# Kernel tuning notes

Hardware: AMD Instinct MI355X
Metric: run time of the kernel (lower is better)

## Reference

```python
import jax, jax.numpy as jnp
import numpy as np

D = 1024          # n_embd
E = 8             # n_experts
FF = 4 * D        # ffn hidden
CAP = 2048        # expert_capacity
W_IMP = 0.01
W_LOAD = 0.01
LAMBDA_Z = 0.001
W_PEN = 0.01
B, S = 4, 2048
T = B * S


def setup_inputs() -> dict:
    key = jax.random.key(0)
    ks = jax.random.split(key, 8)
    x = jax.random.normal(ks[0], (B, S, D), dtype=jnp.float32)
    gate_w = jax.random.normal(ks[1], (E, D), dtype=jnp.float32) * 0.02   # Linear(D,E) weight
    w1 = jax.random.normal(ks[2], (E, D, FF), dtype=jnp.float32) * 0.02   # c_fc weight per expert
    b1 = jnp.zeros((E, FF), dtype=jnp.float32)
    w2 = jax.random.normal(ks[3], (E, FF, D), dtype=jnp.float32) * 0.02   # c_proj weight per expert
    b2 = jnp.zeros((E, D), dtype=jnp.float32)
    rnd = jax.random.uniform(ks[4], (T,), dtype=jnp.float32)              # torch.rand_like(g2)
    return {"x": x, "gate_w": gate_w, "w1": w1, "b1": b1, "w2": w2, "b2": b2, "rnd": rnd}


def _dispatch_ffn_combine(xf, e_ids, pos, wts, mask, w1, b1, w2, b2):
    """Capacity-buffered dispatch -> grouped FFN -> weighted combine for one routing slot.
    xf: [T,D]; e_ids: [T] int; pos: [T] position within expert; wts: [T] combine weight
    (already zeroed where masked); mask: [T] bool within-capacity (and stochastic) mask."""
    pc = jnp.clip(pos, 0, CAP - 1)
    buf = jnp.zeros((E, CAP, xf.shape[-1]), xf.dtype)
    # masked tokens contribute zeros; valid positions are unique per expert so add == set
    buf = buf.at[e_ids, pc].add(xf * mask[:, None].astype(xf.dtype))
    h = jax.nn.gelu(jnp.einsum('ecd,edf->ecf', buf, w1) + b1[:, None, :], approximate=True)
    out = jnp.einsum('ecf,efd->ecd', h, w2) + b2[:, None, :]          # [E,C,D]
    return out[e_ids, pc] * wts[:, None]                               # [T,D]


def _forward(x, gate_w, w1, b1, w2, b2, rnd):
    xf = x.reshape(-1, x.shape[-1])                                    # [T,D]
    logits = xf @ gate_w.T                                             # [T,E] (bias=False)

    # auxiliary losses
    p166 = jax.nn.softmax(logits / 1.66, axis=-1)
    penalty_a = jnp.mean(p166 * (1.0 - p166))
    pm = p166.mean(axis=0)
    penalty_b = 1.0 / E - jnp.mean(pm * (1.0 - pm))
    penalty = W_PEN * (penalty_a + penalty_b)
    z_loss = LAMBDA_Z * jnp.mean(jax.nn.logsumexp(logits, axis=-1) ** 2)

    probs = jax.nn.softmax(logits.astype(jnp.float32), axis=-1).astype(x.dtype)
    weights, sel = jax.lax.top_k(probs, 2)
    g1, g2 = weights[:, 0], weights[:, 1]
    e1, e2 = sel[:, 0], sel[:, 1]
    denom = g1 + g2
    g1n, g2n = g1 / denom, g2 / denom

    oh1 = jax.nn.one_hot(e1, E, dtype=jnp.int32)
    pos1 = jnp.take_along_axis(jnp.cumsum(oh1, axis=0), e1[:, None], axis=1)[:, 0] - 1
    mask1 = pos1 < CAP
    w_slot1 = g1n * mask1.astype(x.dtype)

    oh2 = jax.nn.one_hot(e2, E, dtype=jnp.int32)
    pos2 = jnp.take_along_axis(jnp.cumsum(oh2, axis=0), e2[:, None], axis=1)[:, 0] - 1
    mask2 = (pos2 < CAP) & (rnd < 2.0 * g2n)
    w_slot2 = g2n * mask2.astype(x.dtype)

    # load-balance loss: f_i from top-1 one-hot, P_i from softmax probs
    f_i = oh1.astype(jnp.float32).mean(axis=0)
    P_i = probs.mean(axis=0)
    load_loss = W_LOAD * E * jnp.sum(f_i * P_i)

    # importance loss over combine matrix G (column sums)
    imp = jnp.zeros((E,), x.dtype).at[e1].add(w_slot1).at[e2].add(w_slot2)
    mean = imp.mean()
    var = jnp.var(imp)
    imp_loss = W_IMP * var / (mean ** 2)

    aux = penalty + z_loss + load_loss + imp_loss

    y = _dispatch_ffn_combine(xf, e1, pos1, w_slot1, mask1, w1, b1, w2, b2)
    y = y + _dispatch_ffn_combine(xf, e2, pos2, w_slot2, mask2, w1, b1, w2, b2)
    return y.reshape(x.shape), aux


def reference(x, gate_w, w1, b1, w2, b2, rnd):
    return _forward(x, gate_w, w1, b1, w2, b2, rnd)
```

## Files before the change

kernel.cpp:

```cpp
#include <hip/hip_runtime.h>
#include <math.h>
#include <stdint.h>

#define DD 1024
#define EE 8
#define FF 4096
#define CAPV 2048
#define TT 8192
#define LIST_STRIDE 4096

typedef __bf16 bf16x8 __attribute__((ext_vector_type(8)));
typedef __bf16 bf16x4 __attribute__((ext_vector_type(4)));
typedef float floatx4 __attribute__((ext_vector_type(4)));

typedef __attribute__((address_space(3))) unsigned int as3_uint;
typedef __attribute__((address_space(1))) const unsigned int as1_uint;

__device__ __forceinline__ void gl_lds16(const void* g, void* l) {
    __builtin_amdgcn_global_load_lds((as1_uint*)g, (as3_uint*)l, 16, 0, 0);
}

__device__ __forceinline__ unsigned short f2bf(float f) {
    union { float f; unsigned int u; } v; v.f = f;
    const unsigned int r = v.u + 0x7FFFu + ((v.u >> 16) & 1u);
    return (unsigned short)(r >> 16);
}

__global__ __launch_bounds__(256) void moe_gate_kernel(
    const float* __restrict__ x, const float* __restrict__ gw,
    int* __restrict__ e1o, int* __restrict__ e2o,
    float* __restrict__ g1o, float* __restrict__ g2o,
    float* __restrict__ sums, __bf16* __restrict__ xb)
{
    __shared__ float sgw[EE][DD];
    __shared__ float wp[4][26];
    for (int i = threadIdx.x; i < EE * DD; i += 256) sgw[i >> 10][i & 1023] = gw[i];
    __syncthreads();

    const int wave = threadIdx.x >> 6, lane = threadIdx.x & 63;
    const int gwave = blockIdx.x * 4 + wave;
    const int nwaves = gridDim.x * 4;

    float pa_acc = 0.f, z_acc = 0.f;
    float P_acc[EE] = {0}, p6_acc[EE] = {0};
    int n1_acc[EE] = {0};

    for (int t = gwave; t < TT; t += nwaves) {
        float acc[EE] = {0};
        const float* xr = x + (size_t)t * DD;
        __bf16* xbr = xb + (size_t)t * DD;
        #pragma unroll
        for (int i = 0; i < DD / 64; ++i) {
            const float xv = xr[lane + 64 * i];
            xbr[lane + 64 * i] = (__bf16)xv;
            #pragma unroll
            for (int e = 0; e < EE; ++e) acc[e] += xv * sgw[e][lane + 64 * i];
        }
        #pragma unroll
        for (int e = 0; e < EE; ++e) {
            float v = acc[e];
            #pragma unroll
            for (int off = 32; off > 0; off >>= 1) v += __shfl_xor(v, off, 64);
            acc[e] = v;
        }
        if (lane == 0) {
            float mx = acc[0];
            #pragma unroll
            for (int e = 1; e < EE; ++e) mx = fmaxf(mx, acc[e]);
            float pr[EE], p6[EE], se = 0.f, s6 = 0.f;
            #pragma unroll
            for (int e = 0; e < EE; ++e) {
                pr[e] = __expf(acc[e] - mx); se += pr[e];
                p6[e] = __expf((acc[e] - mx) * (1.0f / 1.66f)); s6 += p6[e];
            }
            const float lse = mx + __logf(se);
            z_acc += lse * lse;
            const float ise = 1.f / se, is6 = 1.f / s6;
            #pragma unroll
            for (int e = 0; e < EE; ++e) {
                pr[e] *= ise; p6[e] *= is6;
                P_acc[e] += pr[e]; p6_acc[e] += p6[e];
                pa_acc += p6[e] * (1.f - p6[e]);
            }
            int a = 0;
            #pragma unroll
            for (int e = 1; e < EE; ++e) if (pr[e] > pr[a]) a = e;
            int b = (a == 0) ? 1 : 0;
            #pragma unroll
            for (int e = 0; e < EE; ++e) if (e != a && pr[e] > pr[b]) b = e;
            n1_acc[a]++;
            const float ga = pr[a], gb = pr[b], idn = 1.f / (ga + gb);
            e1o[t] = a; e2o[t] = b;
            g1o[t] = ga * idn; g2o[t] = gb * idn;
        }
    }
    if (lane == 0) {
        wp[wave][0] = pa_acc; wp[wave][1] = z_acc;
        #pragma unroll
        for (int e = 0; e < EE; ++e) {
            wp[wave][2 + e] = P_acc[e]; wp[wave][10 + e] = p6_acc[e];
            wp[wave][18 + e] = (float)n1_acc[e];
        }
    }
    __syncthreads();
    if (threadIdx.x < 26) {
        const float s = wp[0][threadIdx.x] + wp[1][threadIdx.x] + wp[2][threadIdx.x] + wp[3][threadIdx.x];
        atomicAdd(&sums[threadIdx.x], s);
    }
}

__global__ __launch_bounds__(256) void moe_scan_kernel(
    const int* __restrict__ e1i, const int* __restrict__ e2i,
    const float* __restrict__ g1i, const float* __restrict__ g2i,
    const float* __restrict__ rnd, const float* __restrict__ sums,
    int* __restrict__ etok, int* __restrict__ p1o, int* __restrict__ p2o,
    int* __restrict__ cnt1, int* __restrict__ cnt2,
    float* __restrict__ imp1, float* __restrict__ imp2)
{
    const int bid = blockIdx.x, slot = bid >> 3, e = bid & 7;
    const int tid = threadIdx.x, wave = tid >> 6, lane = tid & 63;
    __shared__ int wtA[4], wtB[4];
    __shared__ float red[256];
    const int* ev = slot ? e2i : e1i;
    const float* gv = slot ? g2i : g1i;
    int* po = slot ? p2o : p1o;
    const int base = slot ? min((int)sums[18 + e], CAPV) : 0;

    int runTot = 0, runM = 0;
    float limp = 0.f;
    for (int c = 0; c < TT / 256; ++c) {
        const int t = c * 256 + tid;
        const int sel = (ev[t] == e) ? 1 : 0;
        const float w = gv[t];
        int ps = sel;
        #pragma unroll
        for (int off = 1; off < 64; off <<= 1) { int v = __shfl_up(ps, off, 64); if (lane >= off) ps += v; }
        if (lane == 63) wtA[wave] = ps;
        __syncthreads();
        int wpre = 0, ctot = 0;
        #pragma unroll
        for (int ww = 0; ww < 4; ++ww) { if (ww < wave) wpre += wtA[ww]; ctot += wtA[ww]; }
        const int pos = runTot + wpre + ps - 1;
        int m, idx;
        if (slot == 0) {
            m = sel && (pos < CAPV);
            idx = pos;
        } else {
            m = (sel && (pos < CAPV) && (rnd[t] < 2.f * w)) ? 1 : 0;
            int pm = m;
            #pragma unroll
            for (int off = 1; off < 64; off <<= 1) { int v = __shfl_up(pm, off, 64); if (lane >= off) pm += v; }
            if (lane == 63) wtB[wave] = pm;
            __syncthreads();
            int wpm = 0, mtot = 0;
            #pragma unroll
            for (int ww = 0; ww < 4; ++ww) { if (ww < wave) wpm += wtB[ww]; mtot += wtB[ww]; }
            idx = runM + wpm + pm - 1;
            runM += mtot;
        }
        if (sel) po[t] = m ? (e * LIST_STRIDE + base + idx) : -1;
        if (m) {
            etok[e * LIST_STRIDE + base + idx] = t;
            limp += w;
        }
        runTot += ctot;
        __syncthreads();
    }
    red[tid] = limp; __syncthreads();
    for (int s = 128; s > 0; s >>= 1) { if (tid < s) red[tid] += red[tid + s]; __syncthreads(); }
    if (tid == 0) {
        if (slot == 0) { cnt1[e] = min(runTot, CAPV); imp1[e] = red[0]; }
        else           { cnt2[e] = runM;              imp2[e] = red[0]; }
    }
}

__global__ void moe_aux_kernel(const float* __restrict__ sums,
                               const float* __restrict__ imp1, const float* __restrict__ imp2,
                               float* __restrict__ out_aux)
{
    if (threadIdx.x != 0 || blockIdx.x != 0) return;
    const float invT = 1.f / (float)TT;
    const float pa = sums[0] / ((float)TT * (float)EE);
    float pb = 0.f, load = 0.f, msum = 0.f;
    float im[EE];
    for (int e = 0; e < EE; ++e) {
        const float pm = sums[10 + e] * invT;
        pb += pm * (1.f - pm);
        load += (sums[18 + e] * invT) * (sums[2 + e] * invT);
        im[e] = imp1[e] + imp2[e];
        msum += im[e];
    }
    pb = 1.f / (float)EE - pb / (float)EE;
    const float penalty = 0.01f * (pa + pb);
    const float z_loss = 0.001f * sums[1] * invT;
    const float load_loss = 0.01f * (float)EE * load;
    const float mean = msum / (float)EE;
    float var = 0.f;
    for (int e = 0; e < EE; ++e) { const float d = im[e] - mean; var += d * d; }
    var /= (float)EE;
    const float imp_loss = 0.01f * var / (mean * mean);
    *out_aux = penalty + z_loss + load_loss + imp_loss;
}

__global__ __launch_bounds__(256) void transpose_bf16_kernel(
    const float* __restrict__ in, __bf16* __restrict__ out, int K, int N)
{
    __shared__ float tile[32][65];
    const int e = blockIdx.z;
    const float* ine = in + (size_t)e * K * N;
    __bf16* oute = out + (size_t)e * K * N;
    const int bk = blockIdx.x * 64, bn = blockIdx.y * 32;
    const int tid = threadIdx.x;
    #pragma unroll
    for (int p = 0; p < 8; ++p) {
        const int idx = p * 256 + tid;
        const int kl = idx >> 5, nl = idx & 31;
        tile[nl][kl] = ine[(size_t)(bk + kl) * N + bn + nl];
    }
    __syncthreads();
    #pragma unroll
    for (int p = 0; p < 4; ++p) {
        const int wdx = p * 256 + tid;
        const int nl = wdx >> 5, c = wdx & 31;
        const unsigned int pk = (unsigned int)f2bf(tile[nl][c * 2])
                              | ((unsigned int)f2bf(tile[nl][c * 2 + 1]) << 16);
        *(unsigned int*)&oute[(size_t)(bn + nl) * K + bk + c * 2] = pk;
    }
}

__global__ __launch_bounds__(512, 2) void moe_ffn1_mfma(
    const __bf16* __restrict__ xb, const __bf16* __restrict__ w1T,
    const float* __restrict__ b1, const int* __restrict__ etok,
    const int* __restrict__ cnt1, const int* __restrict__ cnt2,
    __bf16* __restrict__ H)
{
    const int f = blockIdx.x;
    const int xcd = f & 7, s = f >> 3;
    const int g = xcd * 16 + (s >> 4);
    const int e = g >> 4, n0 = (g & 15) * 256;
    const int m0 = (s & 15) * 256;
    const int ce = cnt1[e] + cnt2[e];
    if (m0 >= ce) return;
    const int tid = threadIdx.x, lane = tid & 63, w = tid >> 6;
    const int wm = w >> 2, wn = w & 3;
    const int quad = lane >> 4, l16 = lane & 15;

    __shared__ __bf16 As[2][16384];
    __shared__ __bf16 Bs[2][16384];

    const int srow = tid >> 3;
    const int srcoff = ((tid & 7) ^ (srow & 7)) * 8;
    const __bf16* ap[4];
    const __bf16* bp[4];
    const __bf16* bbase = w1T + (size_t)e * FF * DD;
    #pragma unroll
    for (int r = 0; r < 4; ++r) {
        const int gr = m0 + r * 64 + srow;
        const int tok = (gr < ce) ? etok[e * LIST_STRIDE + gr] : 0;
        ap[r] = xb + (size_t)tok * DD + srcoff;
        bp[r] = bbase + (size_t)(n0 + r * 64 + srow) * DD + srcoff;
    }
    const int ldst = w * 512;

    floatx4 acc[8][4];
    #pragma unroll
    for (int i = 0; i < 8; ++i)
        #pragma unroll
        for (int j = 0; j < 4; ++j) acc[i][j] = floatx4{0.f, 0.f, 0.f, 0.f};

    const int abase  = (wm * 128 + l16) * 64;
    const int bbase2 = (wn * 64 + l16) * 64;
    const int sw0 = (quad ^ (l16 & 7)) * 8;
    const int sw1 = ((4 + quad) ^ (l16 & 7)) * 8;

    auto stage = [&](int bufi, int koff) {
        #pragma unroll
        for (int r = 0; r < 4; ++r)
            gl_lds16(ap[r] + koff, &As[bufi][r * 4096 + ldst]);
        #pragma unroll
        for (int r = 0; r < 4; ++r)
            gl_lds16(bp[r] + koff, &Bs[bufi][r * 4096 + ldst]);
    };
    auto compute = [&](int bufi) {
        bf16x8 bfr[4][2];
        #pragma unroll
        for (int j = 0; j < 4; ++j) {
            bfr[j][0] = *(const bf16x8*)&Bs[bufi][bbase2 + j * 1024 + sw0];
            bfr[j][1] = *(const bf16x8*)&Bs[bufi][bbase2 + j * 1024 + sw1];
        }
        #pragma unroll
        for (int mh = 0; mh < 2; ++mh) {
            bf16x8 av[4][2];
            #pragma unroll
            for (int i2 = 0; i2 < 4; ++i2) {
                av[i2][0] = *(const bf16x8*)&As[bufi][abase + (mh * 4 + i2) * 1024 + sw0];
                av[i2][1] = *(const bf16x8*)&As[bufi][abase + (mh * 4 + i2) * 1024 + sw1];
            }
            #pragma unroll
            for (int i2 = 0; i2 < 4; ++i2)
                #pragma unroll
                for (int j = 0; j < 4; ++j) {
                    floatx4 c = acc[mh * 4 + i2][j];
                    c = __builtin_amdgcn_mfma_f32_16x16x32_bf16(bfr[j][0], av[i2][0], c, 0, 0, 0);
                    c = __builtin_amdgcn_mfma_f32_16x16x32_bf16(bfr[j][1], av[i2][1], c, 0, 0, 0);
                    acc[mh * 4 + i2][j] = c;
                }
        }
    };

    stage(0, 0);
    stage(1, 64);
    asm volatile("s_waitcnt vmcnt(8)" ::: "memory");
    __builtin_amdgcn_s_barrier();

    #pragma unroll 2
    for (int t = 0; t < 16; ++t) {
        const int cur = t & 1;
        compute(cur);
        asm volatile("s_waitcnt lgkmcnt(0)" ::: "memory");
        __builtin_amdgcn_s_barrier();
        if (t < 14) {
            stage(cur, (t + 2) * 64);
            asm volatile("s_waitcnt vmcnt(8)" ::: "memory");
        } else {
            asm volatile("s_waitcnt vmcnt(0)" ::: "memory");
        }
        __builtin_amdgcn_s_barrier();
    }

    const float* b1e = b1 + (size_t)e * FF;
    #pragma unroll
    for (int i = 0; i < 8; ++i) {
        const int mrow = m0 + wm * 128 + i * 16 + l16;
        __bf16* hrow = H + ((size_t)e * LIST_STRIDE + mrow) * FF;
        #pragma unroll
        for (int j = 0; j < 4; ++j) {
            const int col0 = n0 + wn * 64 + j * 16 + quad * 4;
            const float4 bb = *(const float4*)&b1e[col0];
            float vv[4] = {acc[i][j][0] + bb.x, acc[i][j][1] + bb.y,
                           acc[i][j][2] + bb.z, acc[i][j][3] + bb.w};
            bf16x4 pk;
            #pragma unroll
            for (int r = 0; r < 4; ++r) {
                const float v = vv[r];
                const float u = 0.7978845608028654f * (v + 0.044715f * v * v * v);
                const float th = 1.f - 2.f / (__expf(2.f * u) + 1.f);
                pk[r] = (__bf16)(0.5f * v * (1.f + th));
            }
            *(bf16x4*)&hrow[col0] = pk;
        }
    }
}

__global__ __launch_bounds__(512, 2) void moe_ffn2_mfma(
    const __bf16* __restrict__ H, const __bf16* __restrict__ w2T,
    const float* __restrict__ b2, const int* __restrict__ cnt1,
    const int* __restrict__ cnt2, __bf16* __restrict__ O)
{
    const int f = blockIdx.x;
    const int xcd = f & 7, s = f >> 3;
    const int g = xcd * 4 + (s >> 4);
    const int e = g >> 2, n0 = (g & 3) * 256;
    const int m0 = (s & 15) * 256;
    const int ce = cnt1[e] + cnt2[e];
    if (m0 >= ce) return;
    const int tid = threadIdx.x, lane = tid & 63, w = tid >> 6;
    const int wm = w >> 2, wn = w & 3;
    const int quad = lane >> 4, l16 = lane & 15;

    __shared__ __bf16 As[2][16384];
    __shared__ __bf16 Bs[2][16384];

    const int srow = tid >> 3;
    const int srcoff = ((tid & 7) ^ (srow & 7)) * 8;
    const __bf16* ap[4];
    const __bf16* bp[4];
    const __bf16* bbase = w2T + (size_t)e * DD * FF;
    #pragma unroll
    for (int r = 0; r < 4; ++r) {
        ap[r] = H + ((size_t)e * LIST_STRIDE + m0 + r * 64 + srow) * FF + srcoff;
        bp[r] = bbase + (size_t)(n0 + r * 64 + srow) * FF + srcoff;
    }
    const int ldst = w * 512;

    floatx4 acc[8][4];
    #pragma unroll
    for (int i = 0; i < 8; ++i)
        #pragma unroll
        for (int j = 0; j < 4; ++j) acc[i][j] = floatx4{0.f, 0.f, 0.f, 0.f};

    const int abase  = (wm * 128 + l16) * 64;
    const int bbase2 = (wn * 64 + l16) * 64;
    const int sw0 = (quad ^ (l16 & 7)) * 8;
    const int sw1 = ((4 + quad) ^ (l16 & 7)) * 8;

    auto stage = [&](int bufi, int koff) {
        #pragma unroll
        for (int r = 0; r < 4; ++r)
            gl_lds16(ap[r] + koff, &As[bufi][r * 4096 + ldst]);
        #pragma unroll
        for (int r = 0; r < 4; ++r)
            gl_lds16(bp[r] + koff, &Bs[bufi][r * 4096 + ldst]);
    };
    auto compute = [&](int bufi) {
        bf16x8 bfr[4][2];
        #pragma unroll
        for (int j = 0; j < 4; ++j) {
            bfr[j][0] = *(const bf16x8*)&Bs[bufi][bbase2 + j * 1024 + sw0];
            bfr[j][1] = *(const bf16x8*)&Bs[bufi][bbase2 + j * 1024 + sw1];
        }
        #pragma unroll
        for (int mh = 0; mh < 2; ++mh) {
            bf16x8 av[4][2];
            #pragma unroll
            for (int i2 = 0; i2 < 4; ++i2) {
                av[i2][0] = *(const bf16x8*)&As[bufi][abase + (mh * 4 + i2) * 1024 + sw0];
                av[i2][1] = *(const bf16x8*)&As[bufi][abase + (mh * 4 + i2) * 1024 + sw1];
            }
            #pragma unroll
            for (int i2 = 0; i2 < 4; ++i2)
                #pragma unroll
                for (int j = 0; j < 4; ++j) {
                    floatx4 c = acc[mh * 4 + i2][j];
                    c = __builtin_amdgcn_mfma_f32_16x16x32_bf16(bfr[j][0], av[i2][0], c, 0, 0, 0);
                    c = __builtin_amdgcn_mfma_f32_16x16x32_bf16(bfr[j][1], av[i2][1], c, 0, 0, 0);
                    acc[mh * 4 + i2][j] = c;
                }
        }
    };

    stage(0, 0);
    stage(1, 64);
    asm volatile("s_waitcnt vmcnt(8)" ::: "memory");
    __builtin_amdgcn_s_barrier();

    #pragma unroll 2
    for (int t = 0; t < 64; ++t) {
        const int cur = t & 1;
        compute(cur);
        asm volatile("s_waitcnt lgkmcnt(0)" ::: "memory");
        __builtin_amdgcn_s_barrier();
        if (t < 62) {
            stage(cur, (t + 2) * 64);
            asm volatile("s_waitcnt vmcnt(8)" ::: "memory");
        } else {
            asm volatile("s_waitcnt vmcnt(0)" ::: "memory");
        }
        __builtin_amdgcn_s_barrier();
    }

    const float* b2e = b2 + (size_t)e * DD;
    #pragma unroll
    for (int i = 0; i < 8; ++i) {
        const int grow = m0 + wm * 128 + i * 16 + l16;
        if (grow < ce) {
            __bf16* orow = O + ((size_t)e * LIST_STRIDE + grow) * DD;
            #pragma unroll
            for (int j = 0; j < 4; ++j) {
                const int col0 = n0 + wn * 64 + j * 16 + quad * 4;
                const float4 bb = *(const float4*)&b2e[col0];
                bf16x4 pk;
                pk[0] = (__bf16)(acc[i][j][0] + bb.x);
                pk[1] = (__bf16)(acc[i][j][1] + bb.y);
                pk[2] = (__bf16)(acc[i][j][2] + bb.z);
                pk[3] = (__bf16)(acc[i][j][3] + bb.w);
                *(bf16x4*)&orow[col0] = pk;
            }
        }
    }
}

__global__ __launch_bounds__(256) void moe_combine_kernel(
    const __bf16* __restrict__ O, const float* __restrict__ g1v,
    const float* __restrict__ g2v, const int* __restrict__ p1v,
    const int* __restrict__ p2v, float* __restrict__ y)
{
    const int t = blockIdx.x;
    const int col = threadIdx.x * 4;
    const int p1 = p1v[t], p2 = p2v[t];
    float4 r = make_float4(0.f, 0.f, 0.f, 0.f);
    if (p1 >= 0) {
        const float g = g1v[t];
        const bf16x4 v = *(const bf16x4*)&O[(size_t)p1 * DD + col];
        r.x += g * (float)v[0]; r.y += g * (float)v[1];
        r.z += g * (float)v[2]; r.w += g * (float)v[3];
    }
    if (p2 >= 0) {
        const float g = g2v[t];
        const bf16x4 v = *(const bf16x4*)&O[(size_t)p2 * DD + col];
        r.x += g * (float)v[0]; r.y += g * (float)v[1];
        r.z += g * (float)v[2]; r.w += g * (float)v[3];
    }
    *(float4*)&y[(size_t)t * DD + col] = r;
}

extern "C" void kernel_launch(void* const* d_in, const int* in_sizes, int n_in,
                              void* d_out, int out_size, void* d_ws, size_t ws_size,
                              hipStream_t stream) {
    const float* x   = (const float*)d_in[0];
    const float* gw  = (const float*)d_in[1];
    const float* w1  = (const float*)d_in[2];
    const float* b1  = (const float*)d_in[3];
    const float* w2  = (const float*)d_in[4];
    const float* b2  = (const float*)d_in[5];
    const float* rnd = (const float*)d_in[6];
    float* out = (float*)d_out;

    char* p = (char*)d_ws;
    float* sums = (float*)p;
    float* imp1 = (float*)(p + 128);
    float* imp2 = (float*)(p + 160);
    int*   cnt1 = (int*)(p + 192);
    int*   cnt2 = (int*)(p + 224);
    p += 512;
    int*   e1v = (int*)p;   p += TT * 4;
    int*   e2v = (int*)p;   p += TT * 4;
    float* g1v = (float*)p; p += TT * 4;
    float* g2v = (float*)p; p += TT * 4;
    int*   p1v = (int*)p;   p += TT * 4;
    int*   p2v = (int*)p;   p += TT * 4;
    int*   etok = (int*)p;  p += EE * LIST_STRIDE * 4;
    uintptr_t q = (((uintptr_t)p) + 255) & ~(uintptr_t)255;
    __bf16* xb  = (__bf16*)q;  q += (size_t)TT * DD * 2;
    __bf16* w1T = (__bf16*)q;  q += (size_t)EE * FF * DD * 2;
    __bf16* w2T = (__bf16*)q;  q += (size_t)EE * DD * FF * 2;
    __bf16* H   = (__bf16*)q;  q += (size_t)EE * LIST_STRIDE * FF * 2;
    __bf16* O   = (__bf16*)q;

    hipMemsetAsync(sums, 0, 128, stream);

    moe_gate_kernel<<<256, 256, 0, stream>>>(x, gw, e1v, e2v, g1v, g2v, sums, xb);
    moe_scan_kernel<<<16, 256, 0, stream>>>(e1v, e2v, g1v, g2v, rnd, sums,
                                            etok, p1v, p2v, cnt1, cnt2, imp1, imp2);
    moe_aux_kernel<<<1, 64, 0, stream>>>(sums, imp1, imp2, out + (size_t)TT * DD);

    transpose_bf16_kernel<<<dim3(DD / 64, FF / 32, EE), 256, 0, stream>>>(w1, w1T, DD, FF);
    transpose_bf16_kernel<<<dim3(FF / 64, DD / 32, EE), 256, 0, stream>>>(w2, w2T, FF, DD);

    moe_ffn1_mfma<<<2048, 512, 0, stream>>>(xb, w1T, b1, etok, cnt1, cnt2, H);
    moe_ffn2_mfma<<<512, 512, 0, stream>>>(H, w2T, b2, cnt1, cnt2, O);
    moe_combine_kernel<<<TT, 256, 0, stream>>>(O, g1v, g2v, p1v, p2v, out);
}
```

Baseline: 711.6 us.

## Interleave fine-grained global-to-LDS staging with MFMA sub-phases in FFN K-loops

Replaces the coarse stage-then-compute double-buffered K loop in both expert FFN GEMM kernels with a four-phase schedule. Each phase issues a couple of global_load_lds transfers for the next tiles, loads one K-half of the A/B fragments, and runs 16 MFMAs at raised wave priority (s_setprio). The goal is to spread memory traffic across the compute, keep fewer LDS fragments live, and hide load latency better. It adds many more barriers per iteration and relies on the vmcnt accounting being correct; the clamped tail prefetches issue redundant loads.

```diff
diff --git a/kernel.cpp b/kernel.cpp
--- a/kernel.cpp
+++ b/kernel.cpp
@@ -228,6 +228,91 @@
     }
 }
 
+#define FFN_KLOOP(NT)                                                          \
+                \
+    stA(0,0,0); stA(0,2,0); stB(0,0,0); stB(0,1,0);                            \
+    stA(0,1,0); stA(0,3,0); stB(0,2,0); stB(0,3,0);                            \
+    stA(1,0,1); stA(1,2,1); stB(1,0,1); stB(1,1,1);                            \
+    _Pragma("unroll 2")                                                        \
+    for (int t = 0; t < (NT); ++t) {                                           \
+        const int c = t & 1, o = c ^ 1;                                        \
+        const int u1 = (t + 1 < (NT)) ? t + 1 : (NT) - 1;                      \
+        const int u2 = (t + 2 < (NT)) ? t + 2 : (NT) - 1;                      \
+        bf16x8 bfr[4][2], av[4];                                               \
+                                            \
+        stA(o, 1, u1); stA(o, 3, u1);                                          \
+        asm volatile("s_waitcnt vmcnt(4)" ::: "memory");                       \
+        __builtin_amdgcn_s_barrier();                                          \
+        _Pragma("unroll")                                                      \
+        for (int j = 0; j < 4; ++j)                                            \
+            bfr[j][0] = *(const bf16x8*)&Bs[c][bbase2 + j * 1024 + sw0];       \
+        _Pragma("unroll")                                                      \
+        for (int i = 0; i < 4; ++i)                                            \
+            av[i] = *(const bf16x8*)&As[c][abase + i * 1024 + sw0];            \
+        __builtin_amdgcn_s_setprio(1);                                         \
+        _Pragma("unroll")                                                      \
+        for (int i = 0; i < 4; ++i)                                            \
+            _Pragma("unroll")                                                  \
+            for (int j = 0; j < 4; ++j)                                        \
+                acc[i][j] = __builtin_amdgcn_mfma_f32_16x16x32_bf16(           \
+                    bfr[j][0], av[i], acc[i][j], 0, 0, 0);                     \
+        __builtin_amdgcn_s_setprio(0);                                         \
+        asm volatile("s_waitcnt lgkmcnt(0)" ::: "memory");                     \
+        __builtin_amdgcn_s_barrier();                                          \
+                                            \
+        stB(o, 2, u1); stB(o, 3, u1);                                          \
+        _Pragma("unroll")                                                      \
+        for (int j = 0; j < 4; ++j)                                            \
+            bfr[j][1] = *(const bf16x8*)&Bs[c][bbase2 + j * 1024 + sw1];       \
+        _Pragma("unroll")                                                      \
+        for (int i = 0; i < 4; ++i)                                            \
+            av[i] = *(const bf16x8*)&As[c][abase + i * 1024 + sw1];            \
+        __builtin_amdgcn_s_barrier();                                          \
+        __builtin_amdgcn_s_setprio(1);                                         \
+        _Pragma("unroll")                                                      \
+        for (int i = 0; i < 4; ++i)                                            \
+            _Pragma("unroll")                                                  \
+            for (int j = 0; j < 4; ++j)                                        \
+                acc[i][j] = __builtin_amdgcn_mfma_f32_16x16x32_bf16(           \
+                    bfr[j][1], av[i], acc[i][j], 0, 0, 0);                     \
+        __builtin_amdgcn_s_setprio(0);                                         \
+        asm volatile("s_waitcnt lgkmcnt(0)" ::: "memory");                     \
+        __builtin_amdgcn_s_barrier();        \
+                                            \
+        stA(c, 0, u2); stA(c, 2, u2);                                          \
+        _Pragma("unroll")                                                      \
+        for (int i = 0; i < 4; ++i)                                            \
+            av[i] = *(const bf16x8*)&As[c][abase + (4 + i) * 1024 + sw0];      \
+        __builtin_amdgcn_s_barrier();                                          \
+        __builtin_amdgcn_s_setprio(1);                                         \
+        _Pragma("unroll")                                                      \
+        for (int i = 0; i < 4; ++i)                                            \
+            _Pragma("unroll")                                                  \
+            for (int j = 0; j < 4; ++j)                                        \
+                acc[4 + i][j] = __builtin_amdgcn_mfma_f32_16x16x32_bf16(       \
+                    bfr[j][0], av[i], acc[4 + i][j], 0, 0, 0);                 \
+        __builtin_amdgcn_s_setprio(0);                                         \
+        asm volatile("s_waitcnt lgkmcnt(0)" ::: "memory");                     \
+        __builtin_amdgcn_s_barrier();                                          \
+                                            \
+        stB(c, 0, u2); stB(c, 1, u2);                                          \
+        _Pragma("unroll")                                                      \
+        for (int i = 0; i < 4; ++i)                                            \
+            av[i] = *(const bf16x8*)&As[c][abase + (4 + i) * 1024 + sw1];      \
+        __builtin_amdgcn_s_barrier();                                          \
+        __builtin_amdgcn_s_setprio(1);                                         \
+        _Pragma("unroll")                                                      \
+        for (int i = 0; i < 4; ++i)                                            \
+            _Pragma("unroll")                                                  \
+            for (int j = 0; j < 4; ++j)                                        \
+                acc[4 + i][j] = __builtin_amdgcn_mfma_f32_16x16x32_bf16(       \
+                    bfr[j][1], av[i], acc[4 + i][j], 0, 0, 0);                 \
+        __builtin_amdgcn_s_setprio(0);                                         \
+        asm volatile("s_waitcnt lgkmcnt(0)" ::: "memory");                     \
+        __builtin_amdgcn_s_barrier();                                          \
+    }                                                                          \
+    asm volatile("s_waitcnt vmcnt(0)" ::: "memory");
+
 __global__ __launch_bounds__(512, 2) void moe_ffn1_mfma(
     const __bf16* __restrict__ xb, const __bf16* __restrict__ w1T,
     const float* __restrict__ b1, const int* __restrict__ etok,
@@ -273,60 +358,10 @@
     const int sw0 = (quad ^ (l16 & 7)) * 8;
     const int sw1 = ((4 + quad) ^ (l16 & 7)) * 8;
 
-    auto stage = [&](int bufi, int koff) {
-        #pragma unroll
-        for (int r = 0; r < 4; ++r)
-            gl_lds16(ap[r] + koff, &As[bufi][r * 4096 + ldst]);
-        #pragma unroll
-        for (int r = 0; r < 4; ++r)
-            gl_lds16(bp[r] + koff, &Bs[bufi][r * 4096 + ldst]);
-    };
-    auto compute = [&](int bufi) {
-        bf16x8 bfr[4][2];
-        #pragma unroll
-        for (int j = 0; j < 4; ++j) {
-            bfr[j][0] = *(const bf16x8*)&Bs[bufi][bbase2 + j * 1024 + sw0];
-            bfr[j][1] = *(const bf16x8*)&Bs[bufi][bbase2 + j * 1024 + sw1];
-        }
-        #pragma unroll
-        for (int mh = 0; mh < 2; ++mh) {
-            bf16x8 av[4][2];
-            #pragma unroll
-            for (int i2 = 0; i2 < 4; ++i2) {
-                av[i2][0] = *(const bf16x8*)&As[bufi][abase + (mh * 4 + i2) * 1024 + sw0];
-                av[i2][1] = *(const bf16x8*)&As[bufi][abase + (mh * 4 + i2) * 1024 + sw1];
-            }
-            #pragma unroll
-            for (int i2 = 0; i2 < 4; ++i2)
-                #pragma unroll
-                for (int j = 0; j < 4; ++j) {
-                    floatx4 c = acc[mh * 4 + i2][j];
-                    c = __builtin_amdgcn_mfma_f32_16x16x32_bf16(bfr[j][0], av[i2][0], c, 0, 0, 0);
-                    c = __builtin_amdgcn_mfma_f32_16x16x32_bf16(bfr[j][1], av[i2][1], c, 0, 0, 0);
-                    acc[mh * 4 + i2][j] = c;
-                }
-        }
-    };
-
-    stage(0, 0);
-    stage(1, 64);
-    asm volatile("s_waitcnt vmcnt(8)" ::: "memory");
-    __builtin_amdgcn_s_barrier();
-
-    #pragma unroll 2
-    for (int t = 0; t < 16; ++t) {
-        const int cur = t & 1;
-        compute(cur);
-        asm volatile("s_waitcnt lgkmcnt(0)" ::: "memory");
-        __builtin_amdgcn_s_barrier();
-        if (t < 14) {
-            stage(cur, (t + 2) * 64);
-            asm volatile("s_waitcnt vmcnt(8)" ::: "memory");
-        } else {
-            asm volatile("s_waitcnt vmcnt(0)" ::: "memory");
-        }
-        __builtin_amdgcn_s_barrier();
-    }
+    auto stA = [&](int buf, int r, int u) { gl_lds16(ap[r] + u * 64, &As[buf][r * 4096 + ldst]); };
+    auto stB = [&](int buf, int r, int u) { gl_lds16(bp[r] + u * 64, &Bs[buf][r * 4096 + ldst]); };
+
+    FFN_KLOOP(16)
 
     const float* b1e = b1 + (size_t)e * FF;
     #pragma unroll
@@ -394,60 +429,10 @@
     const int sw0 = (quad ^ (l16 & 7)) * 8;
     const int sw1 = ((4 + quad) ^ (l16 & 7)) * 8;
 
-    auto stage = [&](int bufi, int koff) {
-        #pragma unroll
-        for (int r = 0; r < 4; ++r)
-            gl_lds16(ap[r] + koff, &As[bufi][r * 4096 + ldst]);
-        #pragma unroll
-        for (int r = 0; r < 4; ++r)
-            gl_lds16(bp[r] + koff, &Bs[bufi][r * 4096 + ldst]);
-    };
-    auto compute = [&](int bufi) {
-        bf16x8 bfr[4][2];
-        #pragma unroll
-        for (int j = 0; j < 4; ++j) {
-            bfr[j][0] = *(const bf16x8*)&Bs[bufi][bbase2 + j * 1024 + sw0];
-            bfr[j][1] = *(const bf16x8*)&Bs[bufi][bbase2 + j * 1024 + sw1];
-        }
-        #pragma unroll
-        for (int mh = 0; mh < 2; ++mh) {
-            bf16x8 av[4][2];
-            #pragma unroll
-            for (int i2 = 0; i2 < 4; ++i2) {
-                av[i2][0] = *(const bf16x8*)&As[bufi][abase + (mh * 4 + i2) * 1024 + sw0];
-                av[i2][1] = *(const bf16x8*)&As[bufi][abase + (mh * 4 + i2) * 1024 + sw1];
-            }
-            #pragma unroll
-            for (int i2 = 0; i2 < 4; ++i2)
-                #pragma unroll
-                for (int j = 0; j < 4; ++j) {
-                    floatx4 c = acc[mh * 4 + i2][j];
-                    c = __builtin_amdgcn_mfma_f32_16x16x32_bf16(bfr[j][0], av[i2][0], c, 0, 0, 0);
-                    c = __builtin_amdgcn_mfma_f32_16x16x32_bf16(bfr[j][1], av[i2][1], c, 0, 0, 0);
-                    acc[mh * 4 + i2][j] = c;
-                }
-        }
-    };
-
-    stage(0, 0);
-    stage(1, 64);
-    asm volatile("s_waitcnt vmcnt(8)" ::: "memory");
-    __builtin_amdgcn_s_barrier();
-
-    #pragma unroll 2
-    for (int t = 0; t < 64; ++t) {
-        const int cur = t & 1;
-        compute(cur);
-        asm volatile("s_waitcnt lgkmcnt(0)" ::: "memory");
-        __builtin_amdgcn_s_barrier();
-        if (t < 62) {
-            stage(cur, (t + 2) * 64);
-            asm volatile("s_waitcnt vmcnt(8)" ::: "memory");
-        } else {
-            asm volatile("s_waitcnt vmcnt(0)" ::: "memory");
-        }
-        __builtin_amdgcn_s_barrier();
-    }
+    auto stA = [&](int buf, int r, int u) { gl_lds16(ap[r] + u * 64, &As[buf][r * 4096 + ldst]); };
+    auto stB = [&](int buf, int r, int u) { gl_lds16(bp[r] + u * 64, &Bs[buf][r * 4096 + ldst]); };
+
+    FFN_KLOOP(64)
 
     const float* b2e = b2 + (size_t)e * DD;
     #pragma unroll
```

Result: slower. 746.1 us (+4.8%).

## Switch FFN GEMMs to 32x32x16 MFMA and fuse weight transposes into gate kernel

Applied to the files above, without the earlier changes.

The two expert FFN GEMM kernels now use 32x32x16 bf16 MFMA instructions with floatx16 accumulators instead of pairs of 16x16x32 ops. This roughly halves the LDS fragment loads per FLOP and raises s_setprio around the MFMA bursts. Separately, the gate kernel and both weight transpose kernels are merged into one launch by dispatching on block index, so the transposes can overlap the gating work and two launches go away. The epilogue index mapping is rewritten for the 32x32 output layout, which risks layout bugs, and the larger LDS allocation in the merged kernel may reduce occupancy for the transpose blocks.

```diff
diff --git a/kernel.cpp b/kernel.cpp
--- a/kernel.cpp
+++ b/kernel.cpp
@@ -12,6 +12,7 @@
 typedef __bf16 bf16x8 __attribute__((ext_vector_type(8)));
 typedef __bf16 bf16x4 __attribute__((ext_vector_type(4)));
 typedef float floatx4 __attribute__((ext_vector_type(4)));
+typedef float floatx16 __attribute__((ext_vector_type(16)));
 
 typedef __attribute__((address_space(3))) unsigned int as3_uint;
 typedef __attribute__((address_space(1))) const unsigned int as1_uint;
@@ -26,20 +27,67 @@
     return (unsigned short)(r >> 16);
 }
 
-__global__ __launch_bounds__(256) void moe_gate_kernel(
+#define GATE_BLOCKS 256
+#define T1_BLOCKS 16384
+#define T2_BLOCKS 16384
+
+__device__ __forceinline__ void transpose_body(
+    const float* __restrict__ in, __bf16* __restrict__ out,
+    int K, int N, int bk, int bn, int e, float (*tile)[65], int tid)
+{
+    const float* ine = in + (size_t)e * K * N;
+    __bf16* oute = out + (size_t)e * K * N;
+    #pragma unroll
+    for (int p = 0; p < 8; ++p) {
+        const int idx = p * 256 + tid;
+        const int kl = idx >> 5, nl = idx & 31;
+        tile[nl][kl] = ine[(size_t)(bk + kl) * N + bn + nl];
+    }
+    __syncthreads();
+    #pragma unroll
+    for (int p = 0; p < 4; ++p) {
+        const int wdx = p * 256 + tid;
+        const int nl = wdx >> 5, c = wdx & 31;
+        const unsigned int pk = (unsigned int)f2bf(tile[nl][c * 2])
+                              | ((unsigned int)f2bf(tile[nl][c * 2 + 1]) << 16);
+        *(unsigned int*)&oute[(size_t)(bn + nl) * K + bk + c * 2] = pk;
+    }
+}
+
+__global__ __launch_bounds__(256) void moe_prep_kernel(
     const float* __restrict__ x, const float* __restrict__ gw,
     int* __restrict__ e1o, int* __restrict__ e2o,
     float* __restrict__ g1o, float* __restrict__ g2o,
-    float* __restrict__ sums, __bf16* __restrict__ xb)
-{
-    __shared__ float sgw[EE][DD];
+    float* __restrict__ sums, __bf16* __restrict__ xb,
+    const float* __restrict__ w1, __bf16* __restrict__ w1T,
+    const float* __restrict__ w2, __bf16* __restrict__ w2T)
+{
+    __shared__ float smem[EE * DD];
     __shared__ float wp[4][26];
-    for (int i = threadIdx.x; i < EE * DD; i += 256) sgw[i >> 10][i & 1023] = gw[i];
+    const int bid = blockIdx.x;
+    const int tid = threadIdx.x;
+
+    if (bid >= GATE_BLOCKS) {
+        float (*tile)[65] = (float (*)[65])smem;
+        if (bid < GATE_BLOCKS + T1_BLOCKS) {
+            const int f = bid - GATE_BLOCKS;
+            transpose_body(w1, w1T, DD, FF, (f & 15) * 64, ((f >> 4) & 127) * 32,
+                           f >> 11, tile, tid);
+        } else {
+            const int f = bid - GATE_BLOCKS - T1_BLOCKS;
+            transpose_body(w2, w2T, FF, DD, (f & 63) * 64, ((f >> 6) & 31) * 32,
+                           f >> 11, tile, tid);
+        }
+        return;
+    }
+
+    float (*sgw)[DD] = (float (*)[DD])smem;
+    for (int i = tid; i < EE * DD; i += 256) sgw[i >> 10][i & 1023] = gw[i];
     __syncthreads();
 
-    const int wave = threadIdx.x >> 6, lane = threadIdx.x & 63;
-    const int gwave = blockIdx.x * 4 + wave;
-    const int nwaves = gridDim.x * 4;
+    const int wave = tid >> 6, lane = tid & 63;
+    const int gwave = bid * 4 + wave;
+    const int nwaves = GATE_BLOCKS * 4;
 
     float pa_acc = 0.f, z_acc = 0.f;
     float P_acc[EE] = {0}, p6_acc[EE] = {0};
@@ -103,9 +151,9 @@
         }
     }
     __syncthreads();
-    if (threadIdx.x < 26) {
-        const float s = wp[0][threadIdx.x] + wp[1][threadIdx.x] + wp[2][threadIdx.x] + wp[3][threadIdx.x];
-        atomicAdd(&sums[threadIdx.x], s);
+    if (tid < 26) {
+        const float s = wp[0][tid] + wp[1][tid] + wp[2][tid] + wp[3][tid];
+        atomicAdd(&sums[tid], s);
     }
 }
 
@@ -202,31 +250,42 @@
     *out_aux = penalty + z_loss + load_loss + imp_loss;
 }
 
-__global__ __launch_bounds__(256) void transpose_bf16_kernel(
-    const float* __restrict__ in, __bf16* __restrict__ out, int K, int N)
-{
-    __shared__ float tile[32][65];
-    const int e = blockIdx.z;
-    const float* ine = in + (size_t)e * K * N;
-    __bf16* oute = out + (size_t)e * K * N;
-    const int bk = blockIdx.x * 64, bn = blockIdx.y * 32;
-    const int tid = threadIdx.x;
-    #pragma unroll
-    for (int p = 0; p < 8; ++p) {
-        const int idx = p * 256 + tid;
-        const int kl = idx >> 5, nl = idx & 31;
-        tile[nl][kl] = ine[(size_t)(bk + kl) * N + bn + nl];
-    }
-    __syncthreads();
-    #pragma unroll
-    for (int p = 0; p < 4; ++p) {
-        const int wdx = p * 256 + tid;
-        const int nl = wdx >> 5, c = wdx & 31;
-        const unsigned int pk = (unsigned int)f2bf(tile[nl][c * 2])
-                              | ((unsigned int)f2bf(tile[nl][c * 2 + 1]) << 16);
-        *(unsigned int*)&oute[(size_t)(bn + nl) * K + bk + c * 2] = pk;
-    }
-}
+#define FFN_CORE32(NT)                                                         \
+    stage(0, 0);                                                               \
+    stage(1, 64);                                                              \
+    asm volatile("s_waitcnt vmcnt(8)" ::: "memory");                           \
+    __builtin_amdgcn_s_barrier();                                              \
+    for (int t = 0; t < (NT); ++t) {                                           \
+        const int cur = t & 1;                                                 \
+        _Pragma("unroll")                                                      \
+        for (int ks = 0; ks < 4; ++ks) {                                       \
+            bf16x8 av[4], bv[2];                                               \
+            const int ch = ((ks * 2 + hi) ^ kx) * 8;                           \
+            _Pragma("unroll")                                                  \
+            for (int mi = 0; mi < 4; ++mi)                                     \
+                av[mi] = *(const bf16x8*)&As[cur][ar[mi] + ch];                 \
+            _Pragma("unroll")                                                  \
+            for (int nj = 0; nj < 2; ++nj)                                     \
+                bv[nj] = *(const bf16x8*)&Bs[cur][br[nj] + ch];                 \
+            __builtin_amdgcn_s_setprio(1);                                     \
+            _Pragma("unroll")                                                  \
+            for (int mi = 0; mi < 4; ++mi)                                     \
+                _Pragma("unroll")                                              \
+                for (int nj = 0; nj < 2; ++nj)                                 \
+                    acc[mi][nj] = __builtin_amdgcn_mfma_f32_32x32x16_bf16(     \
+                        bv[nj], av[mi], acc[mi][nj], 0, 0, 0);                 \
+            __builtin_amdgcn_s_setprio(0);                                     \
+        }                                                                      \
+        asm volatile("s_waitcnt lgkmcnt(0)" ::: "memory");                     \
+        __builtin_amdgcn_s_barrier();                                          \
+        if (t < (NT) - 2) {                                                    \
+            stage(cur, (t + 2) * 64);                                          \
+            asm volatile("s_waitcnt vmcnt(8)" ::: "memory");                   \
+        } else {                                                               \
+            asm volatile("s_waitcnt vmcnt(0)" ::: "memory");                   \
+        }                                                                      \
+        __builtin_amdgcn_s_barrier();                                          \
+    }
 
 __global__ __launch_bounds__(512, 2) void moe_ffn1_mfma(
     const __bf16* __restrict__ xb, const __bf16* __restrict__ w1T,
@@ -243,7 +302,8 @@
     if (m0 >= ce) return;
     const int tid = threadIdx.x, lane = tid & 63, w = tid >> 6;
     const int wm = w >> 2, wn = w & 3;
-    const int quad = lane >> 4, l16 = lane & 15;
+    const int l32 = lane & 31, hi = lane >> 5;
+    const int kx = l32 & 7;
 
     __shared__ __bf16 As[2][16384];
     __shared__ __bf16 Bs[2][16384];
@@ -262,16 +322,19 @@
     }
     const int ldst = w * 512;
 
-    floatx4 acc[8][4];
-    #pragma unroll
-    for (int i = 0; i < 8; ++i)
-        #pragma unroll
-        for (int j = 0; j < 4; ++j) acc[i][j] = floatx4{0.f, 0.f, 0.f, 0.f};
-
-    const int abase  = (wm * 128 + l16) * 64;
-    const int bbase2 = (wn * 64 + l16) * 64;
-    const int sw0 = (quad ^ (l16 & 7)) * 8;
-    const int sw1 = ((4 + quad) ^ (l16 & 7)) * 8;
+    floatx16 acc[4][2];
+    #pragma unroll
+    for (int i = 0; i < 4; ++i)
+        #pragma unroll
+        for (int j = 0; j < 2; ++j)
+            #pragma unroll
+            for (int q = 0; q < 16; ++q) acc[i][j][q] = 0.f;
+
+    int ar[4], br[2];
+    #pragma unroll
+    for (int mi = 0; mi < 4; ++mi) ar[mi] = (wm * 128 + mi * 32 + l32) * 64;
+    #pragma unroll
+    for (int nj = 0; nj < 2; ++nj) br[nj] = (wn * 64 + nj * 32 + l32) * 64;
 
     auto stage = [&](int bufi, int koff) {
         #pragma unroll
@@ -281,74 +344,34 @@
         for (int r = 0; r < 4; ++r)
             gl_lds16(bp[r] + koff, &Bs[bufi][r * 4096 + ldst]);
     };
-    auto compute = [&](int bufi) {
-        bf16x8 bfr[4][2];
-        #pragma unroll
-        for (int j = 0; j < 4; ++j) {
-            bfr[j][0] = *(const bf16x8*)&Bs[bufi][bbase2 + j * 1024 + sw0];
-            bfr[j][1] = *(const bf16x8*)&Bs[bufi][bbase2 + j * 1024 + sw1];
-        }
-        #pragma unroll
-        for (int mh = 0; mh < 2; ++mh) {
-            bf16x8 av[4][2];
-            #pragma unroll
-            for (int i2 = 0; i2 < 4; ++i2) {
-                av[i2][0] = *(const bf16x8*)&As[bufi][abase + (mh * 4 + i2) * 1024 + sw0];
-                av[i2][1] = *(const bf16x8*)&As[bufi][abase + (mh * 4 + i2) * 1024 + sw1];
+
+    FFN_CORE32(16)
+
+    const float* b1e = b1 + (size_t)e * FF;
+    #pragma unroll
+    for (int mi = 0; mi < 4; ++mi) {
+        const int mrow = m0 + wm * 128 + mi * 32 + l32;
+        __bf16* hrow = H + ((size_t)e * LIST_STRIDE + mrow) * FF;
+        #pragma unroll
+        for (int nj = 0; nj < 2; ++nj)
+            #pragma unroll
+            for (int rg = 0; rg < 4; ++rg) {
+                const int col0 = n0 + wn * 64 + nj * 32 + rg * 8 + hi * 4;
+                const float4 bb = *(const float4*)&b1e[col0];
+                float vv[4] = {acc[mi][nj][rg * 4 + 0] + bb.x,
+                               acc[mi][nj][rg * 4 + 1] + bb.y,
+                               acc[mi][nj][rg * 4 + 2] + bb.z,
+                               acc[mi][nj][rg * 4 + 3] + bb.w};
+                bf16x4 pk;
+                #pragma unroll
+                for (int r = 0; r < 4; ++r) {
+                    const float v = vv[r];
+                    const float u = 0.7978845608028654f * (v + 0.044715f * v * v * v);
+                    const float th = 1.f - 2.f / (__expf(2.f * u) + 1.f);
+                    pk[r] = (__bf16)(0.5f * v * (1.f + th));
+                }
+                *(bf16x4*)&hrow[col0] = pk;
             }
-            #pragma unroll
-            for (int i2 = 0; i2 < 4; ++i2)
-                #pragma unroll
-                for (int j = 0; j < 4; ++j) {
-                    floatx4 c = acc[mh * 4 + i2][j];
-                    c = __builtin_amdgcn_mfma_f32_16x16x32_bf16(bfr[j][0], av[i2][0], c, 0, 0, 0);
-                    c = __builtin_amdgcn_mfma_f32_16x16x32_bf16(bfr[j][1], av[i2][1], c, 0, 0, 0);
-                    acc[mh * 4 + i2][j] = c;
-                }
-        }
-    };
-
-    stage(0, 0);
-    stage(1, 64);
-    asm volatile("s_waitcnt vmcnt(8)" ::: "memory");
-    __builtin_amdgcn_s_barrier();
-
-    #pragma unroll 2
-    for (int t = 0; t < 16; ++t) {
-        const int cur = t & 1;
-        compute(cur);
-        asm volatile("s_waitcnt lgkmcnt(0)" ::: "memory");
-        __builtin_amdgcn_s_barrier();
-        if (t < 14) {
-            stage(cur, (t + 2) * 64);
-            asm volatile("s_waitcnt vmcnt(8)" ::: "memory");
-        } else {
-            asm volatile("s_waitcnt vmcnt(0)" ::: "memory");
-        }
-        __builtin_amdgcn_s_barrier();
-    }
-
-    const float* b1e = b1 + (size_t)e * FF;
-    #pragma unroll
-    for (int i = 0; i < 8; ++i) {
-        const int mrow = m0 + wm * 128 + i * 16 + l16;
-        __bf16* hrow = H + ((size_t)e * LIST_STRIDE + mrow) * FF;
-        #pragma unroll
-        for (int j = 0; j < 4; ++j) {
-            const int col0 = n0 + wn * 64 + j * 16 + quad * 4;
-            const float4 bb = *(const float4*)&b1e[col0];
-            float vv[4] = {acc[i][j][0] + bb.x, acc[i][j][1] + bb.y,
-                           acc[i][j][2] + bb.z, acc[i][j][3] + bb.w};
-            bf16x4 pk;
-            #pragma unroll
-            for (int r = 0; r < 4; ++r) {
-                const float v = vv[r];
-                const float u = 0.7978845608028654f * (v + 0.044715f * v * v * v);
-                const float th = 1.f - 2.f / (__expf(2.f * u) + 1.f);
-                pk[r] = (__bf16)(0.5f * v * (1.f + th));
-            }
-            *(bf16x4*)&hrow[col0] = pk;
-        }
     }
 }
 
@@ -366,7 +389,8 @@
     if (m0 >= ce) return;
     const int tid = threadIdx.x, lane = tid & 63, w = tid >> 6;
     const int wm = w >> 2, wn = w & 3;
-    const int quad = lane >> 4, l16 = lane & 15;
+    const int l32 = lane & 31, hi = lane >> 5;
+    const int kx = l32 & 7;
 
     __shared__ __bf16 As[2][16384];
     __shared__ __bf16 Bs[2][16384];
@@ -383,16 +407,19 @@
     }
     const int ldst = w * 512;
 
-    floatx4 acc[8][4];
-    #pragma unroll
-    for (int i = 0; i < 8; ++i)
-        #pragma unroll
-        for (int j = 0; j < 4; ++j) acc[i][j] = floatx4{0.f, 0.f, 0.f, 0.f};
-
-    const int abase  = (wm * 128 + l16) * 64;
-    const int bbase2 = (wn * 64 + l16) * 64;
-    const int sw0 = (quad ^ (l16 & 7)) * 8;
-    const int sw1 = ((4 + quad) ^ (l16 & 7)) * 8;
+    floatx16 acc[4][2];
+    #pragma unroll
+    for (int i = 0; i < 4; ++i)
+        #pragma unroll
+        for (int j = 0; j < 2; ++j)
+            #pragma unroll
+            for (int q = 0; q < 16; ++q) acc[i][j][q] = 0.f;
+
+    int ar[4], br[2];
+    #pragma unroll
+    for (int mi = 0; mi < 4; ++mi) ar[mi] = (wm * 128 + mi * 32 + l32) * 64;
+    #pragma unroll
+    for (int nj = 0; nj < 2; ++nj) br[nj] = (wn * 64 + nj * 32 + l32) * 64;
 
     auto stage = [&](int bufi, int koff) {
         #pragma unroll
@@ -402,70 +429,28 @@
         for (int r = 0; r < 4; ++r)
             gl_lds16(bp[r] + koff, &Bs[bufi][r * 4096 + ldst]);
     };
-    auto compute = [&](int bufi) {
-        bf16x8 bfr[4][2];
-        #pragma unroll
-        for (int j = 0; j < 4; ++j) {
-            bfr[j][0] = *(const bf16x8*)&Bs[bufi][bbase2 + j * 1024 + sw0];
-            bfr[j][1] = *(const bf16x8*)&Bs[bufi][bbase2 + j * 1024 + sw1];
-        }
-        #pragma unroll
-        for (int mh = 0; mh < 2; ++mh) {
-            bf16x8 av[4][2];
-            #pragma unroll
-            for (int i2 = 0; i2 < 4; ++i2) {
-                av[i2][0] = *(const bf16x8*)&As[bufi][abase + (mh * 4 + i2) * 1024 + sw0];
-                av[i2][1] = *(const bf16x8*)&As[bufi][abase + (mh * 4 + i2) * 1024 + sw1];
-            }
-            #pragma unroll
-            for (int i2 = 0; i2 < 4; ++i2)
-                #pragma unroll
-                for (int j = 0; j < 4; ++j) {
-                    floatx4 c = acc[mh * 4 + i2][j];
-                    c = __builtin_amdgcn_mfma_f32_16x16x32_bf16(bfr[j][0], av[i2][0], c, 0, 0, 0);
-                    c = __builtin_amdgcn_mfma_f32_16x16x32_bf16(bfr[j][1], av[i2][1], c, 0, 0, 0);
-                    acc[mh * 4 + i2][j] = c;
-                }
-        }
-    };
-
-    stage(0, 0);
-    stage(1, 64);
-    asm volatile("s_waitcnt vmcnt(8)" ::: "memory");
-    __builtin_amdgcn_s_barrier();
-
-    #pragma unroll 2
-    for (int t = 0; t < 64; ++t) {
-        const int cur = t & 1;
-        compute(cur);
-        asm volatile("s_waitcnt lgkmcnt(0)" ::: "memory");
-        __builtin_amdgcn_s_barrier();
-        if (t < 62) {
-            stage(cur, (t + 2) * 64);
-            asm volatile("s_waitcnt vmcnt(8)" ::: "memory");
-        } else {
-            asm volatile("s_waitcnt vmcnt(0)" ::: "memory");
-        }
-        __builtin_amdgcn_s_barrier();
-    }
+
+    FFN_CORE32(64)
 
     const float* b2e = b2 + (size_t)e * DD;
     #pragma unroll
-    for (int i = 0; i < 8; ++i) {
-        const int grow = m0 + wm * 128 + i * 16 + l16;
+    for (int mi = 0; mi < 4; ++mi) {
+        const int grow = m0 + wm * 128 + mi * 32 + l32;
         if (grow < ce) {
             __bf16* orow = O + ((size_t)e * LIST_STRIDE + grow) * DD;
             #pragma unroll
-            for (int j = 0; j < 4; ++j) {
-                const int col0 = n0 + wn * 64 + j * 16 + quad * 4;
-                const float4 bb = *(const float4*)&b2e[col0];
-                bf16x4 pk;
-                pk[0] = (__bf16)(acc[i][j][0] + bb.x);
-                pk[1] = (__bf16)(acc[i][j][1] + bb.y);
-                pk[2] = (__bf16)(acc[i][j][2] + bb.z);
-                pk[3] = (__bf16)(acc[i][j][3] + bb.w);
-                *(bf16x4*)&orow[col0] = pk;
-            }
+            for (int nj = 0; nj < 2; ++nj)
+                #pragma unroll
+                for (int rg = 0; rg < 4; ++rg) {
+                    const int col0 = n0 + wn * 64 + nj * 32 + rg * 8 + hi * 4;
+                    const float4 bb = *(const float4*)&b2e[col0];
+                    bf16x4 pk;
+                    pk[0] = (__bf16)(acc[mi][nj][rg * 4 + 0] + bb.x);
+                    pk[1] = (__bf16)(acc[mi][nj][rg * 4 + 1] + bb.y);
+                    pk[2] = (__bf16)(acc[mi][nj][rg * 4 + 2] + bb.z);
+                    pk[3] = (__bf16)(acc[mi][nj][rg * 4 + 3] + bb.w);
+                    *(bf16x4*)&orow[col0] = pk;
+                }
         }
     }
 }
@@ -529,14 +514,12 @@
 
     hipMemsetAsync(sums, 0, 128, stream);
 
-    moe_gate_kernel<<<256, 256, 0, stream>>>(x, gw, e1v, e2v, g1v, g2v, sums, xb);
+    moe_prep_kernel<<<GATE_BLOCKS + T1_BLOCKS + T2_BLOCKS, 256, 0, stream>>>(
+        x, gw, e1v, e2v, g1v, g2v, sums, xb, w1, w1T, w2, w2T);
     moe_scan_kernel<<<16, 256, 0, stream>>>(e1v, e2v, g1v, g2v, rnd, sums,
                                             etok, p1v, p2v, cnt1, cnt2, imp1, imp2);
     moe_aux_kernel<<<1, 64, 0, stream>>>(sums, imp1, imp2, out + (size_t)TT * DD);
 
-    transpose_bf16_kernel<<<dim3(DD / 64, FF / 32, EE), 256, 0, stream>>>(w1, w1T, DD, FF);
-    transpose_bf16_kernel<<<dim3(FF / 64, DD / 32, EE), 256, 0, stream>>>(w2, w2T, FF, DD);
-
     moe_ffn1_mfma<<<2048, 512, 0, stream>>>(xb, w1T, b1, etok, cnt1, cnt2, H);
     moe_ffn2_mfma<<<512, 512, 0, stream>>>(H, w2T, b2, cnt1, cnt2, O);
     moe_combine_kernel<<<TT, 256, 0, stream>>>(O, g1v, g2v, p1v, p2v, out);
```

Measured after the change: 764.9 us. 7.5% more time.
